# Performance work log

Hardware: AMD Instinct MI355X
Metric: run time of the kernel (lower is better)

## Reference

```python
import jax, jax.numpy as jnp
import numpy as np

B, C, L = 4, 64, 4096
RED = 4          # reduction -> q/k channels = C // RED = 16
N_HASHES = 4
HASH_BUCKETS = min(L // 4, 32)  # = 32, matches torch code
EPS = 1e-5


def _conv1x1(x, W, b):
    # x: [B, Cin, L], W: [Cout, Cin], b: [Cout]
    return jnp.einsum('bcl,oc->bol', x, W) + b[None, :, None]


def setup_inputs() -> dict:
    key = jax.random.key(0)
    ks = jax.random.split(key, 12)
    Cq = C // RED
    x = jax.random.normal(ks[0], (B, C, L), dtype=jnp.float32)
    hash_idx = jax.random.randint(ks[1], (B, N_HASHES, L), 0, HASH_BUCKETS, dtype=jnp.int32)
    sC = 1.0 / np.sqrt(C)
    Wq = jax.random.normal(ks[2], (Cq, C), dtype=jnp.float32) * sC
    bq = jax.random.normal(ks[3], (Cq,), dtype=jnp.float32) * 0.01
    Wk = jax.random.normal(ks[4], (Cq, C), dtype=jnp.float32) * sC
    bk = jax.random.normal(ks[5], (Cq,), dtype=jnp.float32) * 0.01
    Wv = jax.random.normal(ks[6], (C, C), dtype=jnp.float32) * sC
    bv = jax.random.normal(ks[7], (C,), dtype=jnp.float32) * 0.01
    Wo = jax.random.normal(ks[8], (C, C), dtype=jnp.float32) * sC
    bo = jax.random.normal(ks[9], (C,), dtype=jnp.float32) * 0.01
    gamma = jax.random.normal(ks[10], (1,), dtype=jnp.float32)  # nonzero so attn path matters
    bn_w = jnp.ones((C,), dtype=jnp.float32)
    bn_b = jnp.zeros((C,), dtype=jnp.float32)
    return dict(x=x, hash_idx=hash_idx, Wq=Wq, bq=bq, Wk=Wk, bk=bk,
                Wv=Wv, bv=bv, Wo=Wo, bo=bo, gamma=gamma, bn_w=bn_w, bn_b=bn_b)


def reference(x, hash_idx, Wq, bq, Wk, bk, Wv, bv, Wo, bo, gamma, bn_w, bn_b):
    # 1x1 conv projections
    q = _conv1x1(x, Wq, bq)   # [B, C/RED, L]
    k = _conv1x1(x, Wk, bk)   # [B, C/RED, L]
    v = _conv1x1(x, Wv, bv)   # [B, C, L]

    qT = q.transpose(0, 2, 1)  # [B, L, Cq]
    kT = k.transpose(0, 2, 1)
    vT = v.transpose(0, 2, 1)  # [B, L, C]

    # raw scores are hash-independent; only the bucket mask changes per hash
    scores = jnp.einsum('bic,bjc->bij', qT, kT)  # [B, L, L], no sqrt(d) scaling (matches torch)

    n_hashes = hash_idx.shape[1]
    acc = jnp.zeros_like(vT)
    for h in range(n_hashes):  # small fixed loop
        idx = hash_idx[:, h, :]                       # [B, L]
        mask = idx[:, :, None] == idx[:, None, :]     # same-bucket mask [B, L, L]
        s = jnp.where(mask, scores, -1e9)
        attn = jax.nn.softmax(s, axis=-1)             # within-bucket softmax (diag always valid)
        acc = acc + jnp.einsum('bij,bjc->bic', attn, vT)
    attn_out = (acc / n_hashes).transpose(0, 2, 1)    # [B, C, L], averaged over hashes

    out = _conv1x1(attn_out, Wo, bo)
    out = gamma * out + x                             # residual with learned scalar

    # BatchNorm1d, training mode: biased batch stats over (B, L) per channel
    mean = out.mean(axis=(0, 2), keepdims=True)
    var = out.var(axis=(0, 2), keepdims=True)
    out = (out - mean) * jax.lax.rsqrt(var + EPS)
    out = out * bn_w[None, :, None] + bn_b[None, :, None]
    return out
```

## Files before the change

kernel.cpp:

```cpp
#include <hip/hip_runtime.h>
#include <math.h>

#define Bn 4
#define Cn 64
#define Ln 4096
#define CQ 16
#define NH 4
#define NB 32
#define EPSV 1e-5f

#define MAXS 384
#define SFULL 192

#define QSZ   (Bn*Ln*CQ)
#define VSZ   (Bn*Ln*Cn)
#define ACCSZ (Bn*Ln*Cn)
#define NBH   (Bn*NH)

#define OFF_K   QSZ
#define OFF_V   (2*QSZ)
#define OFF_ACC (2*QSZ + VSZ)

#define LOG2E 1.44269504088896f
#define WSTR 36

__global__ __launch_bounds__(256) void proj_kernel(
        const float* __restrict__ x,
        const float* __restrict__ Wq, const float* __restrict__ bq,
        const float* __restrict__ Wk, const float* __restrict__ bk,
        const float* __restrict__ Wv, const float* __restrict__ bv,
        float* __restrict__ q, float* __restrict__ k, float* __restrict__ v) {
    __shared__ float sWt[Cn*WSTR];
    __shared__ float sb[32];
    int tid = threadIdx.x;
    int third = blockIdx.x % 3;
    int pg    = blockIdx.x / 3;
    int rbase = third * 32;
    for (int idx = tid; idx < 32*Cn; idx += 256) {
        int c = idx & 63, rr = idx >> 6;
        int r = rbase + rr;
        float w;
        if (r < 16)      w = Wq[r*Cn + c];
        else if (r < 32) w = Wk[(r-16)*Cn + c];
        else             w = Wv[(r-32)*Cn + c];
        sWt[c*WSTR + rr] = w;
    }
    if (tid < 32) {
        int r = rbase + tid;
        sb[tid] = (r < 16) ? bq[r] : (r < 32 ? bk[r-16] : bv[r-32]);
    }
    __syncthreads();
    int p = tid & 63, og = tid >> 6;
    int gp = pg * 64 + p;
    int b = gp >> 12, l = gp & (Ln - 1);
    const float* xp = &x[b*Cn*Ln + l];
    int rr0 = og * 8;
    float val[8];
    #pragma unroll
    for (int i = 0; i < 8; i++) val[i] = sb[rr0 + i];
    #pragma unroll
    for (int c0 = 0; c0 < Cn; c0 += 8) {
        float xv[8];
        #pragma unroll
        for (int i = 0; i < 8; i++) xv[i] = xp[(c0 + i)*Ln];
        #pragma unroll
        for (int i = 0; i < 8; i++) {
            const float4 wa = *(const float4*)&sWt[(c0 + i)*WSTR + rr0];
            const float4 wb = *(const float4*)&sWt[(c0 + i)*WSTR + rr0 + 4];
            float xvi = xv[i];
            val[0] = fmaf(wa.x, xvi, val[0]); val[1] = fmaf(wa.y, xvi, val[1]);
            val[2] = fmaf(wa.z, xvi, val[2]); val[3] = fmaf(wa.w, xvi, val[3]);
            val[4] = fmaf(wb.x, xvi, val[4]); val[5] = fmaf(wb.y, xvi, val[5]);
            val[6] = fmaf(wb.z, xvi, val[6]); val[7] = fmaf(wb.w, xvi, val[7]);
        }
    }
    int f = third*8 + og*2;
    float4 t0 = make_float4(val[0], val[1], val[2], val[3]);
    float4 t1 = make_float4(val[4], val[5], val[6], val[7]);
    float4* q4 = (float4*)&q[gp*CQ];
    float4* k4 = (float4*)&k[gp*CQ];
    float4* v4 = (float4*)&v[gp*Cn];
    if (f < 4)      { q4[f]   = t0; q4[f+1] = t1; }
    else if (f < 8) { k4[f-4] = t0; k4[f-3] = t1; }
    else            { v4[f-8] = t0; v4[f-7] = t1; }
}

__device__ __forceinline__ float quad_reduce_sum(float d) {
    d += __int_as_float(__builtin_amdgcn_mov_dpp(__float_as_int(d), 0xB1, 0xF, 0xF, true));
    d += __int_as_float(__builtin_amdgcn_mov_dpp(__float_as_int(d), 0x4E, 0xF, 0xF, true));
    return d;
}

__device__ __forceinline__ float rowsum16(float x) {
    x += __int_as_float(__builtin_amdgcn_mov_dpp(__float_as_int(x), 0x114, 0xF, 0xF, true));
    x += __int_as_float(__builtin_amdgcn_mov_dpp(__float_as_int(x), 0x118, 0xF, 0xF, true));
    return x;
}

template<int NS> struct Sweep {
    float4 qr[NS];
    float4 o[NS][4];
    float  lsum[NS];
    int    ir[NS];
};

template<int NS>
__device__ __forceinline__ void sweep_init(Sweep<NS>& st, int q0, int S, int act,
        const int* list, const float4* Q4, int qq, int c4) {
    #pragma unroll
    for (int s = 0; s < NS; s++) {
        int qi = q0 + s*4 + qq;
        int a = act && (qi < S);
        st.ir[s] = a ? list[qi] : -1;
        float4 t = make_float4(0.f, 0.f, 0.f, 0.f);
        if (a) {
            t = Q4[(size_t)st.ir[s]*4 + c4];
            t.x *= LOG2E; t.y *= LOG2E; t.z *= LOG2E; t.w *= LOG2E;
        }
        st.qr[s] = t;
        st.lsum[s] = 0.f;
        #pragma unroll
        for (int tt = 0; tt < 4; tt++) st.o[s][tt] = make_float4(0.f, 0.f, 0.f, 0.f);
    }
}

template<int NS, bool MASKED>
__device__ __forceinline__ void kb_step(Sweep<NS>& st, int kb, int nkv,
        const float4* ks4, const float4* vs4, int l15, int kk,
        int i0, int i1, int i2, int i3) {
    const float4 kq = ks4[kb*16 + l15];
    const float4 va = vs4[kb*64 + i0*16 + l15];
    const float4 vb = vs4[kb*64 + i1*16 + l15];
    const float4 vc = vs4[kb*64 + i2*16 + l15];
    const float4 vd = vs4[kb*64 + i3*16 + l15];
    #pragma unroll
    for (int s = 0; s < NS; s++) {
        float d = st.qr[s].x * kq.x;
        d = fmaf(st.qr[s].y, kq.y, d);
        d = fmaf(st.qr[s].z, kq.z, d);
        d = fmaf(st.qr[s].w, kq.w, d);
        d = quad_reduce_sum(d);
        float pw = __builtin_amdgcn_exp2f(d);
        if (MASKED) pw = ((kb*4 + kk) < nkv) ? pw : 0.f;
        st.lsum[s] += pw;
        st.o[s][0].x = fmaf(pw, va.x, st.o[s][0].x); st.o[s][0].y = fmaf(pw, va.y, st.o[s][0].y);
        st.o[s][0].z = fmaf(pw, va.z, st.o[s][0].z); st.o[s][0].w = fmaf(pw, va.w, st.o[s][0].w);
        st.o[s][1].x = fmaf(pw, vb.x, st.o[s][1].x); st.o[s][1].y = fmaf(pw, vb.y, st.o[s][1].y);
        st.o[s][1].z = fmaf(pw, vb.z, st.o[s][1].z); st.o[s][1].w = fmaf(pw, vb.w, st.o[s][1].w);
        st.o[s][2].x = fmaf(pw, vc.x, st.o[s][2].x); st.o[s][2].y = fmaf(pw, vc.y, st.o[s][2].y);
        st.o[s][2].z = fmaf(pw, vc.z, st.o[s][2].z); st.o[s][2].w = fmaf(pw, vc.w, st.o[s][2].w);
        st.o[s][3].x = fmaf(pw, vd.x, st.o[s][3].x); st.o[s][3].y = fmaf(pw, vd.y, st.o[s][3].y);
        st.o[s][3].z = fmaf(pw, vd.z, st.o[s][3].z); st.o[s][3].w = fmaf(pw, vd.w, st.o[s][3].w);
    }
}

template<int NS>
__device__ __forceinline__ void sweep_keys(Sweep<NS>& st, int nk,
        const float4* ks4, const float4* vs4, int l15, int kk,
        int i0, int i1, int i2, int i3) {
    int nf = nk >> 2;
    for (int kb = 0; kb < nf; kb++)
        kb_step<NS,false>(st, kb, nk, ks4, vs4, l15, kk, i0, i1, i2, i3);
    if (nk & 3)
        kb_step<NS,true>(st, nf, nk, ks4, vs4, l15, kk, i0, i1, i2, i3);
}

template<int NS, int MODE>
__device__ __forceinline__ void sweep_fin(Sweep<NS>& st, float* __restrict__ acc,
        int b, int h, int qq, int lane, int c4) {
    #pragma unroll
    for (int s = 0; s < NS; s++) {
        st.lsum[s] = rowsum16(st.lsum[s]);
        #pragma unroll
        for (int t = 0; t < 4; t++) {
            st.o[s][t].x = rowsum16(st.o[s][t].x);
            st.o[s][t].y = rowsum16(st.o[s][t].y);
            st.o[s][t].z = rowsum16(st.o[s][t].z);
            st.o[s][t].w = rowsum16(st.o[s][t].w);
        }
    }
    if ((lane & 15) < 12) return;
    #pragma unroll
    for (int s = 0; s < NS; s++) {
        if (st.ir[s] >= 0) {
            float inv = 1.f / st.lsum[s];
            #pragma unroll
            for (int t = 0; t < 4; t++) {
                float4 r;
                r.x = st.o[s][t].x * inv; r.y = st.o[s][t].y * inv;
                r.z = st.o[s][t].z * inv; r.w = st.o[s][t].w * inv;
                int ch = ((qq + t) & 3)*16 + c4*4;
                if (MODE == 1) {
                    *(float4*)&acc[(((size_t)h*Bn + b)*Ln + st.ir[s])*Cn + ch] = r;
                } else {
                    float* ap = &acc[((size_t)b*Ln + st.ir[s])*Cn + ch];
                    atomicAdd(&ap[0], r.x); atomicAdd(&ap[1], r.y);
                    atomicAdd(&ap[2], r.z); atomicAdd(&ap[3], r.w);
                }
            }
        }
    }
}

template<int NS, int MODE>
__device__ __forceinline__ void run_sweep(int q0, int S, int act,
        const int* list, const float4* Q4,
        const float4* ks4, const float4* vs4, float* __restrict__ acc,
        int b, int h, int qq, int lane, int c4, int l15, int kk,
        int i0, int i1, int i2, int i3) {
    Sweep<NS> st;
    sweep_init<NS>(st, q0, S, act, list, Q4, qq, c4);
    sweep_keys<NS>(st, S, ks4, vs4, l15, kk, i0, i1, i2, i3);
    sweep_fin<NS,MODE>(st, acc, b, h, qq, lane, c4);
}

__device__ __forceinline__ void stage_kv(int tid, int nk, int k0, const int* list,
        const float4* K4, const float4* V4, float4* ks4, float4* vs4) {
    const float4 z = make_float4(0.f, 0.f, 0.f, 0.f);
    int nb4 = (nk + 3) >> 2;
    for (int G = tid; G < nb4*16; G += 512) {
        int j = G >> 2;
        ks4[G] = (j < nk) ? K4[(size_t)list[k0 + j]*4 + (G & 3)] : z;
    }
    for (int F = tid; F < nb4*64; F += 512) {
        int kb = F >> 6, ii = (F >> 4) & 3, k2 = (F >> 2) & 3, cc = F & 3;
        int j = kb*4 + k2;
        vs4[F] = (j < nk) ? V4[(size_t)list[k0 + j]*16 + ii*4 + cc] : z;
    }
}

template<int MODE>
__global__ __launch_bounds__(512, 2) void attn_kernel(
        const float* __restrict__ q, const float* __restrict__ k,
        const float* __restrict__ v, const int* __restrict__ hidx,
        float* __restrict__ acc) {
    __shared__ int list[MAXS];
    __shared__ int wtot[8];
    __shared__ float4 ks4[SFULL*4];
    __shared__ float4 vs4[SFULL*16];
    int blk = blockIdx.x;
    int u  = blk & (NB-1);
    int bh = blk >> 5;
    int b  = bh >> 2;
    int h  = bh & 3;
    int tid = threadIdx.x;

    const int4* hp4 = (const int4*)&hidx[bh*Ln + tid*8];
    int hv[8];
    #pragma unroll
    for (int t = 0; t < 2; t++) {
        int4 tmp = hp4[t];
        hv[t*4+0]=tmp.x; hv[t*4+1]=tmp.y; hv[t*4+2]=tmp.z; hv[t*4+3]=tmp.w;
    }
    int myCnt = 0;
    #pragma unroll
    for (int t = 0; t < 8; t++) myCnt += (hv[t] == u);
    int lane = tid & 63, wv = tid >> 6;
    int pre = myCnt;
    #pragma unroll
    for (int d = 1; d < 64; d <<= 1) {
        int t = __shfl_up(pre, d, 64);
        if (lane >= d) pre += t;
    }
    if (lane == 63) wtot[wv] = pre;
    __syncthreads();
    int base = 0, Sall = 0;
    #pragma unroll
    for (int w = 0; w < 8; w++) {
        base += (w < wv) ? wtot[w] : 0;
        Sall += wtot[w];
    }
    int S = min(Sall, MAXS);
    int excl = base + pre - myCnt;
    #pragma unroll
    for (int t = 0; t < 8; t++) {
        if (hv[t] == u) {
            if (excl < MAXS) list[excl] = tid*8 + t;
            excl++;
        }
    }
    __syncthreads();

    int qq = (lane >> 4) & 3;
    int kk = (lane >> 2) & 3;
    int c4 = lane & 3;
    int l15 = lane & 15;
    int i0 = qq, i1 = (qq+1)&3, i2 = (qq+2)&3, i3 = (qq+3)&3;
    const float4* Q4 = (const float4*)&q[(size_t)b*Ln*CQ];
    const float4* K4 = (const float4*)&k[(size_t)b*Ln*CQ];
    const float4* V4 = (const float4*)&v[(size_t)b*Ln*Cn];

    if (S <= SFULL) {
        stage_kv(tid, S, 0, list, K4, V4, ks4, vs4);
        __syncthreads();
        if (wv*16 < S)
            run_sweep<4,MODE>(wv*16, S, 1, list, Q4, ks4, vs4, acc,
                              b, h, qq, lane, c4, l15, kk, i0, i1, i2, i3);
        for (int qb = 128 + wv*4; qb < S; qb += 32)
            run_sweep<1,MODE>(qb, S, 1, list, Q4, ks4, vs4, acc,
                              b, h, qq, lane, c4, l15, kk, i0, i1, i2, i3);
    } else {
        for (int q0s = 0; q0s < S; q0s += 128) {
            int q0 = q0s + wv*16;
            int act = q0 < S;
            Sweep<4> st;
            sweep_init<4>(st, q0, S, act, list, Q4, qq, c4);
            for (int k0 = 0; k0 < S; k0 += SFULL) {
                int nk = min(SFULL, S - k0);
                __syncthreads();
                stage_kv(tid, nk, k0, list, K4, V4, ks4, vs4);
                __syncthreads();
                if (act) sweep_keys<4>(st, nk, ks4, vs4, l15, kk, i0, i1, i2, i3);
            }
            if (act) sweep_fin<4,MODE>(st, acc, b, h, qq, lane, c4);
        }
    }
}

#define OSTR 68

template<int MODE>
__global__ __launch_bounds__(256) void outconv_kernel(
        const float* __restrict__ acc, const float* __restrict__ Wo,
        const float* __restrict__ bo, const float* __restrict__ gamma,
        const float* __restrict__ x, float* __restrict__ y) {
    __shared__ float sWt[Cn*OSTR];
    __shared__ float sA[Cn*33];
    __shared__ float sb[Cn];
    int tid = threadIdx.x;
    int pg = blockIdx.x;
    for (int idx = tid; idx < Cn*Cn; idx += 256) {
        int c = idx & 63, o = idx >> 6;
        sWt[c*OSTR + o] = Wo[o*Cn + c];
    }
    if (tid < Cn) sb[tid] = bo[tid];
    const float4* a4 = (const float4*)&acc[(size_t)pg*32*Cn];
    #pragma unroll
    for (int r = 0; r < 2; r++) {
        int idx = r*256 + tid;
        int p = idx >> 4, c0 = (idx & 15) * 4;
        float4 t = a4[idx];
        if (MODE == 1) {
            float4 t1 = a4[(size_t)ACCSZ/4   + idx];
            float4 t2 = a4[(size_t)ACCSZ/4*2 + idx];
            float4 t3 = a4[(size_t)ACCSZ/4*3 + idx];
            t.x += t1.x + t2.x + t3.x; t.y += t1.y + t2.y + t3.y;
            t.z += t1.z + t2.z + t3.z; t.w += t1.w + t2.w + t3.w;
        }
        sA[(c0+0)*33 + p] = t.x*0.25f;
        sA[(c0+1)*33 + p] = t.y*0.25f;
        sA[(c0+2)*33 + p] = t.z*0.25f;
        sA[(c0+3)*33 + p] = t.w*0.25f;
    }
    __syncthreads();
    float g = gamma[0];
    int p = tid & 31, og = tid >> 5;
    int gp = pg * 32 + p;
    int b = gp >> 12, l = gp & (Ln - 1);
    int o0 = og * 8;
    float val[8];
    #pragma unroll
    for (int i = 0; i < 8; i++) val[i] = sb[o0 + i];
    #pragma unroll
    for (int c = 0; c < Cn; c++) {
        float av = sA[c*33 + p];
        const float4 wa = *(const float4*)&sWt[c*OSTR + o0];
        const float4 wb = *(const float4*)&sWt[c*OSTR + o0 + 4];
        val[0] = fmaf(wa.x, av, val[0]); val[1] = fmaf(wa.y, av, val[1]);
        val[2] = fmaf(wa.z, av, val[2]); val[3] = fmaf(wa.w, av, val[3]);
        val[4] = fmaf(wb.x, av, val[4]); val[5] = fmaf(wb.y, av, val[5]);
        val[6] = fmaf(wb.z, av, val[6]); val[7] = fmaf(wb.w, av, val[7]);
    }
    #pragma unroll
    for (int i = 0; i < 8; i++) {
        int o = o0 + i;
        float yv = fmaf(g, val[i], x[(b*Cn + o)*Ln + l]);
        y[(b*Cn + o)*Ln + l] = yv;
    }
}

__global__ __launch_bounds__(256) void stats_kernel(
        const float* __restrict__ y, float* __restrict__ ssumP, float* __restrict__ ssqP) {
    int c = blockIdx.x >> 2;
    int part = blockIdx.x & 3;
    int tid = threadIdx.x;
    const float4* yp = (const float4*)&y[(part*Cn + c)*Ln];
    float s = 0.f, s2 = 0.f;
    #pragma unroll
    for (int i = 0; i < 4; i++) {
        float4 t = yp[i*256 + tid];
        s  += t.x + t.y + t.z + t.w;
        s2 += t.x*t.x + t.y*t.y + t.z*t.z + t.w*t.w;
    }
    #pragma unroll
    for (int w = 1; w < 64; w <<= 1) {
        s  += __shfl_xor(s,  w, 64);
        s2 += __shfl_xor(s2, w, 64);
    }
    __shared__ float rs[4], rs2[4];
    int wv = tid >> 6;
    if ((tid & 63) == 0) { rs[wv] = s; rs2[wv] = s2; }
    __syncthreads();
    if (tid == 0) {
        ssumP[blockIdx.x] = rs[0]+rs[1]+rs[2]+rs[3];
        ssqP[blockIdx.x]  = rs2[0]+rs2[1]+rs2[2]+rs2[3];
    }
}

__global__ __launch_bounds__(256) void norm_kernel(
        const float* __restrict__ y,
        const float* __restrict__ ssumP, const float* __restrict__ ssqP,
        const float* __restrict__ bnw, const float* __restrict__ bnb,
        float* __restrict__ out) {
    int idx = blockIdx.x * 256 + threadIdx.x;
    int flat = idx * 4;
    int c = (flat >> 12) & 63;
    float s = 0.f, s2 = 0.f;
    #pragma unroll
    for (int hh = 0; hh < 4; hh++) { s += ssumP[c*4+hh]; s2 += ssqP[c*4+hh]; }
    const float n = (float)(Bn*Ln);
    float mu = s / n;
    float var = s2 / n - mu*mu;
    float is = rsqrtf(var + EPSV);
    float w = is * bnw[c];
    float bb = bnb[c] - mu * w;
    float4 t = ((const float4*)y)[idx];
    float4 r;
    r.x = t.x*w + bb; r.y = t.y*w + bb; r.z = t.z*w + bb; r.w = t.w*w + bb;
    ((float4*)out)[idx] = r;
}

extern "C" void kernel_launch(void* const* d_in, const int* in_sizes, int n_in,
                              void* d_out, int out_size, void* d_ws, size_t ws_size,
                              hipStream_t stream) {
    const float* x    = (const float*)d_in[0];
    const int*   hidx = (const int*)  d_in[1];
    const float* Wq   = (const float*)d_in[2];
    const float* bq   = (const float*)d_in[3];
    const float* Wk   = (const float*)d_in[4];
    const float* bk   = (const float*)d_in[5];
    const float* Wv   = (const float*)d_in[6];
    const float* bv   = (const float*)d_in[7];
    const float* Wo   = (const float*)d_in[8];
    const float* bo   = (const float*)d_in[9];
    const float* gam  = (const float*)d_in[10];
    const float* bnw  = (const float*)d_in[11];
    const float* bnb  = (const float*)d_in[12];
    float* out = (float*)d_out;

    float* ws  = (float*)d_ws;
    float* q   = ws;
    float* k   = ws + OFF_K;
    float* v   = ws + OFF_V;
    float* acc = ws + OFF_ACC;
    float* y   = ws;

    const size_t bigNeed = ((size_t)OFF_ACC + 4*(size_t)ACCSZ + 512) * sizeof(float);
    bool big = ws_size >= bigNeed;
    float* ssumP = acc + (big ? 4*(size_t)ACCSZ : (size_t)ACCSZ);
    float* ssqP  = ssumP + 256;

    proj_kernel<<<Bn*Ln/64*3, 256, 0, stream>>>(x, Wq, bq, Wk, bk, Wv, bv, q, k, v);
    if (big) {
        attn_kernel<1><<<NBH*NB, 512, 0, stream>>>(q, k, v, hidx, acc);
        outconv_kernel<1><<<Bn*Ln/32, 256, 0, stream>>>(acc, Wo, bo, gam, x, y);
    } else {
        hipMemsetAsync(acc, 0, (size_t)ACCSZ*sizeof(float), stream);
        attn_kernel<0><<<NBH*NB, 512, 0, stream>>>(q, k, v, hidx, acc);
        outconv_kernel<0><<<Bn*Ln/32, 256, 0, stream>>>(acc, Wo, bo, gam, x, y);
    }
    stats_kernel<<<Cn*4, 256, 0, stream>>>(y, ssumP, ssqP);
    norm_kernel<<<Bn*Cn*Ln/4/256, 256, 0, stream>>>(y, ssumP, ssqP, bnw, bnb, out);
}
```

Measured before the change: 152.2 us.

## Fuse output conv, BatchNorm stats and normalize via grid-wide atomic barrier

Merges the output 1x1 conv, the BatchNorm statistics kernel and the normalize kernel into one persistent launch of 256 blocks. Each block writes per-channel partial sums, then all blocks wait on an atomic counter (reset inside proj_kernel) before reducing the stats and writing normalized output straight from registers. This removes the intermediate y round trip through global memory and two kernel launches. In exchange it relies on all 256 blocks being co-resident for the spin barrier, and each block now does a redundant global reduction over the partials.

```diff
diff --git a/kernel.cpp b/kernel.cpp
--- a/kernel.cpp
+++ b/kernel.cpp
@@ -23,16 +23,21 @@
 
 #define LOG2E 1.44269504088896f
 #define WSTR 36
+#define OSTR 68
+#define NBLK_F 256
+#define FPOS 64
 
 __global__ __launch_bounds__(256) void proj_kernel(
         const float* __restrict__ x,
         const float* __restrict__ Wq, const float* __restrict__ bq,
         const float* __restrict__ Wk, const float* __restrict__ bk,
         const float* __restrict__ Wv, const float* __restrict__ bv,
-        float* __restrict__ q, float* __restrict__ k, float* __restrict__ v) {
+        float* __restrict__ q, float* __restrict__ k, float* __restrict__ v,
+        int* __restrict__ cnt) {
     __shared__ float sWt[Cn*WSTR];
     __shared__ float sb[32];
     int tid = threadIdx.x;
+    if (blockIdx.x == 0 && tid == 0) *cnt = 0;
     int third = blockIdx.x % 3;
     int pg    = blockIdx.x / 3;
     int rbase = third * 32;
@@ -317,27 +322,31 @@
     }
 }
 
-#define OSTR 68
-
 template<int MODE>
-__global__ __launch_bounds__(256) void outconv_kernel(
+__global__ __launch_bounds__(512, 1) void fused_out_kernel(
         const float* __restrict__ acc, const float* __restrict__ Wo,
         const float* __restrict__ bo, const float* __restrict__ gamma,
-        const float* __restrict__ x, float* __restrict__ y) {
+        const float* __restrict__ x,
+        const float* __restrict__ bnw, const float* __restrict__ bnb,
+        float* __restrict__ out,
+        float* __restrict__ Psum, float* __restrict__ Psq,
+        int* __restrict__ cnt) {
     __shared__ float sWt[Cn*OSTR];
-    __shared__ float sA[Cn*33];
+    __shared__ float sA[Cn*OSTR];
     __shared__ float sb[Cn];
+    __shared__ float sred[512], sred2[512];
+    __shared__ float swv[Cn], sbb[Cn];
     int tid = threadIdx.x;
     int pg = blockIdx.x;
-    for (int idx = tid; idx < Cn*Cn; idx += 256) {
+    for (int idx = tid; idx < Cn*Cn; idx += 512) {
         int c = idx & 63, o = idx >> 6;
         sWt[c*OSTR + o] = Wo[o*Cn + c];
     }
     if (tid < Cn) sb[tid] = bo[tid];
-    const float4* a4 = (const float4*)&acc[(size_t)pg*32*Cn];
+    const float4* a4 = (const float4*)&acc[(size_t)pg*FPOS*Cn];
     #pragma unroll
     for (int r = 0; r < 2; r++) {
-        int idx = r*256 + tid;
+        int idx = r*512 + tid;
         int p = idx >> 4, c0 = (idx & 15) * 4;
         float4 t = a4[idx];
         if (MODE == 1) {
@@ -347,15 +356,15 @@
             t.x += t1.x + t2.x + t3.x; t.y += t1.y + t2.y + t3.y;
             t.z += t1.z + t2.z + t3.z; t.w += t1.w + t2.w + t3.w;
         }
-        sA[(c0+0)*33 + p] = t.x*0.25f;
-        sA[(c0+1)*33 + p] = t.y*0.25f;
-        sA[(c0+2)*33 + p] = t.z*0.25f;
-        sA[(c0+3)*33 + p] = t.w*0.25f;
+        sA[(c0+0)*OSTR + p] = t.x*0.25f;
+        sA[(c0+1)*OSTR + p] = t.y*0.25f;
+        sA[(c0+2)*OSTR + p] = t.z*0.25f;
+        sA[(c0+3)*OSTR + p] = t.w*0.25f;
     }
     __syncthreads();
     float g = gamma[0];
-    int p = tid & 31, og = tid >> 5;
-    int gp = pg * 32 + p;
+    int p = tid & 63, og = tid >> 6;
+    int gp = pg * FPOS + p;
     int b = gp >> 12, l = gp & (Ln - 1);
     int o0 = og * 8;
     float val[8];
@@ -363,7 +372,7 @@
     for (int i = 0; i < 8; i++) val[i] = sb[o0 + i];
     #pragma unroll
     for (int c = 0; c < Cn; c++) {
-        float av = sA[c*33 + p];
+        float av = sA[c*OSTR + p];
         const float4 wa = *(const float4*)&sWt[c*OSTR + o0];
         const float4 wb = *(const float4*)&sWt[c*OSTR + o0 + 4];
         val[0] = fmaf(wa.x, av, val[0]); val[1] = fmaf(wa.y, av, val[1]);
@@ -371,63 +380,60 @@
         val[4] = fmaf(wb.x, av, val[4]); val[5] = fmaf(wb.y, av, val[5]);
         val[6] = fmaf(wb.z, av, val[6]); val[7] = fmaf(wb.w, av, val[7]);
     }
+    float yv8[8];
+    #pragma unroll
+    for (int i = 0; i < 8; i++)
+        yv8[i] = fmaf(g, val[i], x[((size_t)b*Cn + o0 + i)*Ln + l]);
+    __syncthreads();
+    #pragma unroll
+    for (int i = 0; i < 8; i++) sA[(o0+i)*OSTR + p] = yv8[i];
+    __syncthreads();
+    if (tid < Cn) {
+        float s = 0.f, s2 = 0.f;
+        for (int pp = 0; pp < FPOS; pp++) {
+            float yv = sA[tid*OSTR + pp];
+            s += yv;
+            s2 = fmaf(yv, yv, s2);
+        }
+        Psum[tid*NBLK_F + pg] = s;
+        Psq [tid*NBLK_F + pg] = s2;
+    }
+    __threadfence();
+    __syncthreads();
+    if (tid == 0) {
+        __hip_atomic_fetch_add(cnt, 1, __ATOMIC_ACQ_REL, __HIP_MEMORY_SCOPE_AGENT);
+        while (__hip_atomic_load(cnt, __ATOMIC_ACQUIRE, __HIP_MEMORY_SCOPE_AGENT) < NBLK_F)
+            __builtin_amdgcn_s_sleep(8);
+    }
+    __syncthreads();
+    {
+        int c = tid >> 3, j = tid & 7;
+        const float* ps = &Psum[c*NBLK_F + j*32];
+        const float* pq = &Psq [c*NBLK_F + j*32];
+        float s = 0.f, s2 = 0.f;
+        #pragma unroll 8
+        for (int i = 0; i < 32; i++) { s += ps[i]; s2 += pq[i]; }
+        sred[tid] = s; sred2[tid] = s2;
+    }
+    __syncthreads();
+    if (tid < Cn) {
+        float s = 0.f, s2 = 0.f;
+        #pragma unroll
+        for (int j = 0; j < 8; j++) { s += sred[tid*8 + j]; s2 += sred2[tid*8 + j]; }
+        const float n = (float)(Bn*Ln);
+        float mu = s / n;
+        float var = s2 / n - mu*mu;
+        float is = rsqrtf(var + EPSV);
+        float w = is * bnw[tid];
+        swv[tid] = w;
+        sbb[tid] = bnb[tid] - mu * w;
+    }
+    __syncthreads();
     #pragma unroll
     for (int i = 0; i < 8; i++) {
         int o = o0 + i;
-        float yv = fmaf(g, val[i], x[(b*Cn + o)*Ln + l]);
-        y[(b*Cn + o)*Ln + l] = yv;
-    }
-}
-
-__global__ __launch_bounds__(256) void stats_kernel(
-        const float* __restrict__ y, float* __restrict__ ssumP, float* __restrict__ ssqP) {
-    int c = blockIdx.x >> 2;
-    int part = blockIdx.x & 3;
-    int tid = threadIdx.x;
-    const float4* yp = (const float4*)&y[(part*Cn + c)*Ln];
-    float s = 0.f, s2 = 0.f;
-    #pragma unroll
-    for (int i = 0; i < 4; i++) {
-        float4 t = yp[i*256 + tid];
-        s  += t.x + t.y + t.z + t.w;
-        s2 += t.x*t.x + t.y*t.y + t.z*t.z + t.w*t.w;
-    }
-    #pragma unroll
-    for (int w = 1; w < 64; w <<= 1) {
-        s  += __shfl_xor(s,  w, 64);
-        s2 += __shfl_xor(s2, w, 64);
-    }
-    __shared__ float rs[4], rs2[4];
-    int wv = tid >> 6;
-    if ((tid & 63) == 0) { rs[wv] = s; rs2[wv] = s2; }
-    __syncthreads();
-    if (tid == 0) {
-        ssumP[blockIdx.x] = rs[0]+rs[1]+rs[2]+rs[3];
-        ssqP[blockIdx.x]  = rs2[0]+rs2[1]+rs2[2]+rs2[3];
-    }
-}
-
-__global__ __launch_bounds__(256) void norm_kernel(
-        const float* __restrict__ y,
-        const float* __restrict__ ssumP, const float* __restrict__ ssqP,
-        const float* __restrict__ bnw, const float* __restrict__ bnb,
-        float* __restrict__ out) {
-    int idx = blockIdx.x * 256 + threadIdx.x;
-    int flat = idx * 4;
-    int c = (flat >> 12) & 63;
-    float s = 0.f, s2 = 0.f;
-    #pragma unroll
-    for (int hh = 0; hh < 4; hh++) { s += ssumP[c*4+hh]; s2 += ssqP[c*4+hh]; }
-    const float n = (float)(Bn*Ln);
-    float mu = s / n;
-    float var = s2 / n - mu*mu;
-    float is = rsqrtf(var + EPSV);
-    float w = is * bnw[c];
-    float bb = bnb[c] - mu * w;
-    float4 t = ((const float4*)y)[idx];
-    float4 r;
-    r.x = t.x*w + bb; r.y = t.y*w + bb; r.z = t.z*w + bb; r.w = t.w*w + bb;
-    ((float4*)out)[idx] = r;
+        out[((size_t)b*Cn + o)*Ln + l] = fmaf(yv8[i], swv[o], sbb[o]);
+    }
 }
 
 extern "C" void kernel_launch(void* const* d_in, const int* in_sizes, int n_in,
@@ -453,22 +459,24 @@
     float* k   = ws + OFF_K;
     float* v   = ws + OFF_V;
     float* acc = ws + OFF_ACC;
-    float* y   = ws;
-
-    const size_t bigNeed = ((size_t)OFF_ACC + 4*(size_t)ACCSZ + 512) * sizeof(float);
+
+    const size_t bigNeed = ((size_t)OFF_ACC + 4*(size_t)ACCSZ
+                            + 2*(size_t)Cn*NBLK_F + 16) * sizeof(float);
     bool big = ws_size >= bigNeed;
-    float* ssumP = acc + (big ? 4*(size_t)ACCSZ : (size_t)ACCSZ);
-    float* ssqP  = ssumP + 256;
-
-    proj_kernel<<<Bn*Ln/64*3, 256, 0, stream>>>(x, Wq, bq, Wk, bk, Wv, bv, q, k, v);
+    size_t accN = big ? 4*(size_t)ACCSZ : (size_t)ACCSZ;
+    float* Psum = acc + accN;
+    float* Psq  = Psum + (size_t)Cn*NBLK_F;
+    int*   cnt  = (int*)(Psq + (size_t)Cn*NBLK_F);
+
+    proj_kernel<<<Bn*Ln/64*3, 256, 0, stream>>>(x, Wq, bq, Wk, bk, Wv, bv, q, k, v, cnt);
     if (big) {
         attn_kernel<1><<<NBH*NB, 512, 0, stream>>>(q, k, v, hidx, acc);
-        outconv_kernel<1><<<Bn*Ln/32, 256, 0, stream>>>(acc, Wo, bo, gam, x, y);
+        fused_out_kernel<1><<<NBLK_F, 512, 0, stream>>>(acc, Wo, bo, gam, x,
+                                                        bnw, bnb, out, Psum, Psq, cnt);
     } else {
         hipMemsetAsync(acc, 0, (size_t)ACCSZ*sizeof(float), stream);
         attn_kernel<0><<<NBH*NB, 512, 0, stream>>>(q, k, v, hidx, acc);
-        outconv_kernel<0><<<Bn*Ln/32, 256, 0, stream>>>(acc, Wo, bo, gam, x, y);
-    }
-    stats_kernel<<<Cn*4, 256, 0, stream>>>(y, ssumP, ssqP);
-    norm_kernel<<<Bn*Cn*Ln/4/256, 256, 0, stream>>>(y, ssumP, ssqP, bnw, bnb, out);
-}
+        fused_out_kernel<0><<<NBLK_F, 512, 0, stream>>>(acc, Wo, bo, gam, x,
+                                                        bnw, bnb, out, Psum, Psq, cnt);
+    }
+}
```

Result: slower. 202.9 us (+33.3%).
